# Performance work log

Measured on AMD Instinct MI355X. Metric: run time of the kernel, lower is better.

The kernel has to match this reference:

```python
import jax, jax.numpy as jnp
import numpy as np
import math

HEADS = 16
HEAD_DIM = 64
MODEL_DIM = HEADS * HEAD_DIM
SEQ = 2048
BATCH = 2


def setup_inputs() -> dict:
    key = jax.random.key(0)
    ks = jax.random.split(key, 11)
    s = 0.02
    return {
        "query": jax.random.normal(ks[0], (SEQ, BATCH, MODEL_DIM), jnp.float32),
        "key": jax.random.normal(ks[1], (SEQ, BATCH, MODEL_DIM), jnp.float32),
        "value": jax.random.normal(ks[2], (SEQ, BATCH, MODEL_DIM), jnp.float32),
        "mask": jnp.ones((1, SEQ, 1), jnp.int32),
        "Wq": jax.random.normal(ks[3], (MODEL_DIM, MODEL_DIM), jnp.float32) * s,
        "bq": jax.random.normal(ks[4], (MODEL_DIM,), jnp.float32) * s,
        "Wk": jax.random.normal(ks[5], (MODEL_DIM, MODEL_DIM), jnp.float32) * s,
        "bk": jax.random.normal(ks[6], (MODEL_DIM,), jnp.float32) * s,
        "Wv": jax.random.normal(ks[7], (MODEL_DIM, MODEL_DIM), jnp.float32) * s,
        "bv": jax.random.normal(ks[8], (MODEL_DIM,), jnp.float32) * s,
        "Wo": jax.random.normal(ks[9], (MODEL_DIM, MODEL_DIM), jnp.float32) * s,
        "bo": jax.random.normal(ks[10], (MODEL_DIM,), jnp.float32) * s,
    }


def _proj(x, W, b):
    # torch nn.Linear: y = x @ W.T + b ; then view to [.., H, D]
    y = jnp.einsum("sbm,nm->sbn", x, W) + b
    return y.reshape(x.shape[0], x.shape[1], HEADS, HEAD_DIM)


def reference(query, key, value, mask, Wq, bq, Wk, bk, Wv, bv, Wo, bo):
    # NOTE: original module applies mask to `score` AFTER softmax has been
    # taken, and the masked score is discarded -> mask has no effect.
    del mask
    seq_len, batch_size, _ = query.shape
    scale = 1.0 / math.sqrt(HEAD_DIM)
    q = _proj(query, Wq, bq)   # [S,B,H,D]
    k = _proj(key, Wk, bk)
    v = _proj(value, Wv, bv)
    score = jnp.einsum("ibhd,jbhd->ijbh", q, k) * scale  # [S,S,B,H]
    attn = jax.nn.softmax(score, axis=1)  # softmax over key axis j
    # dropout: eval-mode identity (deterministic baseline)
    x = jnp.einsum("ijbh,jbhd->ibhd", attn, v)
    x = x.reshape(seq_len, batch_size, MODEL_DIM)
    return jnp.einsum("sbm,nm->sbn", x, Wo) + bo
```

## Files before the change

### kernel.cpp

```cpp
#include <hip/hip_runtime.h>

#define SEQ    2048
#define NBATCH 2
#define NHEAD  16
#define HD     64
#define MD     1024
#define TOK    (SEQ * NBATCH)
#define WN8    (MD * MD / 8)

typedef __attribute__((ext_vector_type(4)))  float f32x4;
typedef __attribute__((ext_vector_type(16))) float f32x16;
typedef __attribute__((ext_vector_type(8)))  short bf16x8;
typedef __attribute__((ext_vector_type(8)))  unsigned short u16x8;

__device__ __forceinline__ unsigned short f2bf(float f) {
  union { float f; unsigned int u; } x; x.f = f;
  unsigned int u = x.u + 0x7fffu + ((x.u >> 16) & 1u);
  return (unsigned short)(u >> 16);
}

__device__ __forceinline__ unsigned cvtpk(float lo, float hi) {
  unsigned r;
  asm("v_cvt_pk_bf16_f32 %0, %1, %2" : "=v"(r) : "v"(lo), "v"(hi));
  return r;
}
__device__ __forceinline__ void plswap(unsigned &a, unsigned &b) {
  asm volatile("v_permlane32_swap_b32 %0, %1" : "+v"(a), "+v"(b));
}

__device__ __forceinline__ void gload_lds16(const void* g, void* l) {
  typedef const __attribute__((address_space(1))) unsigned int* gp_t;
  typedef __attribute__((address_space(3))) unsigned int* lp_t;
  __builtin_amdgcn_global_load_lds((gp_t)g, (lp_t)l, 16, 0, 0);
}

__global__ __launch_bounds__(256) void cvt_w(
    const float* __restrict__ wq, const float* __restrict__ wk,
    const float* __restrict__ wv, const float* __restrict__ wo,
    unsigned short* __restrict__ owq, unsigned short* __restrict__ owk,
    unsigned short* __restrict__ owv, unsigned short* __restrict__ owo) {
  const int i = blockIdx.x * 256 + threadIdx.x;
  const int s = i >> 17;
  const int r = i & (WN8 - 1);
  const float* src = s == 0 ? wq : (s == 1 ? wk : (s == 2 ? wv : wo));
  unsigned short* dst = s == 0 ? owq : (s == 1 ? owk : (s == 2 ? owv : owo));
  const float4* p = (const float4*)src + (size_t)r * 2;
  float4 a = p[0];
  float4 b = p[1];
  u16x8 o;
  o[0] = f2bf(a.x); o[1] = f2bf(a.y); o[2] = f2bf(a.z); o[3] = f2bf(a.w);
  o[4] = f2bf(b.x); o[5] = f2bf(b.y); o[6] = f2bf(b.z); o[7] = f2bf(b.w);
  *((u16x8*)dst + r) = o;
}

__global__ __launch_bounds__(512) void gemm_qkv(
    const float* __restrict__ Xq, const float* __restrict__ Xk,
    const float* __restrict__ Xv, const unsigned short* __restrict__ Wq,
    const unsigned short* __restrict__ Wk, const unsigned short* __restrict__ Wv,
    const float* __restrict__ bq, const float* __restrict__ bk, const float* __restrict__ bv,
    unsigned short* __restrict__ Qo, unsigned short* __restrict__ Ko,
    unsigned short* __restrict__ Vo, float qscale) {
  __shared__ unsigned short sA[3][128 * 32];
  __shared__ unsigned short sB[3][128 * 32];
  const int tid  = threadIdx.x;
  const int lane = tid & 63;
  const int wave = tid >> 6;
  const int wm   = (wave >> 2) << 6;
  const int wn   = (wave & 3) << 5;
  const int l15  = lane & 15;
  const int g    = lane >> 4;

  const int flat = blockIdx.x + (blockIdx.y << 3) + (blockIdx.z << 8);
  const int nx   = (flat & 63) >> 3;
  const int gr   = ((flat >> 6) << 3) + (flat & 7);
  const int ny   = gr & 31;
  const int z    = gr >> 5;

  const float* Xf; const unsigned short* Wb; const float* bias;
  if (z == 0)      { Xf = Xq; Wb = Wq; bias = bq; }
  else if (z == 1) { Xf = Xk; Wb = Wk; bias = bk; }
  else             { Xf = Xv; Wb = Wv; bias = bv; }
  int bM, bN;
  if (z < 2) { bM = ny << 7; bN = nx << 7; }
  else       { bM = nx << 7; bN = ny << 7; }
  const int bX = (z < 2) ? bM : bN;
  const int bW = (z < 2) ? bN : bM;
  unsigned short* sX3 = (z < 2) ? &sA[0][0] : &sB[0][0];
  unsigned short* sW3 = (z < 2) ? &sB[0][0] : &sA[0][0];

  f32x4 acc[4][2];
#pragma unroll
  for (int a_ = 0; a_ < 4; ++a_)
#pragma unroll
    for (int b_ = 0; b_ < 2; ++b_)
      acc[a_][b_] = f32x4{0.f, 0.f, 0.f, 0.f};

  const int r = tid >> 2, cc = tid & 3;
  const float* xsrc = Xf + (size_t)(bX + r) * MD + cc * 8;
  const unsigned short* wsrc = Wb + (size_t)(bW + r) * MD + cc * 8;

  float4 ra0, rb0, ra1, rb1;
  auto xissue0 = [&](int kt) {
    ra0 = *(const float4*)(xsrc + (kt << 5));
    rb0 = *(const float4*)(xsrc + (kt << 5) + 4);
  };
  auto xissue1 = [&](int kt) {
    ra1 = *(const float4*)(xsrc + (kt << 5));
    rb1 = *(const float4*)(xsrc + (kt << 5) + 4);
  };
  auto xwrite0 = [&](int c) {
    union { unsigned u[4]; bf16x8 v; } w;
    w.u[0] = cvtpk(ra0.x, ra0.y); w.u[1] = cvtpk(ra0.z, ra0.w);
    w.u[2] = cvtpk(rb0.x, rb0.y); w.u[3] = cvtpk(rb0.z, rb0.w);
    *(bf16x8*)(sX3 + c * 4096 + tid * 8) = w.v;
  };
  auto xwrite1 = [&](int c) {
    union { unsigned u[4]; bf16x8 v; } w;
    w.u[0] = cvtpk(ra1.x, ra1.y); w.u[1] = cvtpk(ra1.z, ra1.w);
    w.u[2] = cvtpk(rb1.x, rb1.y); w.u[3] = cvtpk(rb1.z, rb1.w);
    *(bf16x8*)(sX3 + c * 4096 + tid * 8) = w.v;
  };
  auto wissue = [&](int c, int kt) {
    gload_lds16(wsrc + (kt << 5), (char*)(sW3 + c * 4096) + tid * 16);
  };

  auto mfma_step = [&](int c) {
    bf16x8 af[4], bfr[2];
#pragma unroll
    for (int f = 0; f < 4; ++f)
      af[f] = *(const bf16x8*)&sA[c][(wm + f * 16 + l15) * 32 + g * 8];
#pragma unroll
    for (int f = 0; f < 2; ++f)
      bfr[f] = *(const bf16x8*)&sB[c][(wn + f * 16 + l15) * 32 + g * 8];
#pragma unroll
    for (int mf = 0; mf < 4; ++mf)
#pragma unroll
      for (int nf = 0; nf < 2; ++nf)
        acc[mf][nf] = __builtin_amdgcn_mfma_f32_16x16x32_bf16(af[mf], bfr[nf], acc[mf][nf], 0, 0, 0);
  };

  const int nk = MD >> 5;
  auto endwait = [&](int e) {
    if (e + 4 < nk)      asm volatile("s_waitcnt vmcnt(3)" ::: "memory");
    else if (e + 2 < nk) asm volatile("s_waitcnt vmcnt(1)" ::: "memory");
    else                 asm volatile("s_waitcnt vmcnt(0)" ::: "memory");
    asm volatile("s_waitcnt lgkmcnt(0)" ::: "memory");
    __builtin_amdgcn_s_barrier();
  };

  xissue0(0);
  xissue1(1);
  wissue(0, 0);
  wissue(1, 1);
  asm volatile("s_waitcnt vmcnt(4)" ::: "memory");
  xwrite0(0);
  asm volatile("s_waitcnt vmcnt(2)" ::: "memory");
  xwrite1(1);
  xissue0(2);
  xissue1(3);
  asm volatile("s_waitcnt vmcnt(4)" ::: "memory");
  asm volatile("s_waitcnt lgkmcnt(0)" ::: "memory");
  __builtin_amdgcn_s_barrier();

  for (int kt = 0; kt < nk; kt += 2) {
    if (kt + 2 < nk) { xwrite0((kt + 2) % 3); wissue((kt + 2) % 3, kt + 2); }
    if (kt + 4 < nk) xissue0(kt + 4);
    mfma_step(kt % 3);
    endwait(kt);
    if (kt + 3 < nk) { xwrite1((kt + 3) % 3); wissue((kt + 3) % 3, kt + 3); }
    if (kt + 5 < nk) xissue1(kt + 5);
    mfma_step((kt + 1) % 3);
    if (kt + 2 < nk) endwait(kt + 1);
  }

  if (z < 2) {
    unsigned short* O = (z == 0) ? Qo : Ko;
    const float scale = (z == 0) ? qscale : 1.0f;
#pragma unroll
    for (int nf = 0; nf < 2; ++nf) {
      const int cch = bN + wn + nf * 16 + l15;
      const float bb = bias[cch];
      const int h = cch >> 6, d = cch & 63;
#pragma unroll
      for (int mf = 0; mf < 4; ++mf)
#pragma unroll
        for (int i = 0; i < 4; ++i) {
          const int t = bM + wm + mf * 16 + (g << 2) + i;
          const int b = t & 1, s = t >> 1;
          O[((((b << 4) + h) * SEQ + s) << 6) + d] = f2bf((acc[mf][nf][i] + bb) * scale);
        }
    }
  } else {
#pragma unroll
    for (int mf = 0; mf < 4; ++mf)
#pragma unroll
      for (int i = 0; i < 4; ++i) {
        const int rch = bM + wm + mf * 16 + (g << 2) + i;
        const float bb = bias[rch];
        const int h = rch >> 6, d = rch & 63;
#pragma unroll
        for (int nf = 0; nf < 2; ++nf) {
          const int t = bN + wn + nf * 16 + l15;
          const int b = t & 1, s = t >> 1;
          Vo[((((b << 4) + h) << 6) + d) * SEQ + s] = f2bf(acc[mf][nf][i] + bb);
        }
      }
  }
}

__global__ __launch_bounds__(512) void gemm_oproj(const unsigned short* __restrict__ A,
                                                  const unsigned short* __restrict__ B,
                                                  const float* __restrict__ bias,
                                                  float* __restrict__ O) {
  __shared__ unsigned short sA[3][128 * 32];
  __shared__ unsigned short sB[3][128 * 32];
  const int tid  = threadIdx.x;
  const int lane = tid & 63;
  const int wave = tid >> 6;
  const int wm   = (wave >> 2) << 6;
  const int wn   = (wave & 3) << 5;
  const int l15  = lane & 15;
  const int g    = lane >> 4;

  const int flat = blockIdx.x + (blockIdx.y << 3);
  const int nx   = (flat & 63) >> 3;
  const int gr   = ((flat >> 6) << 3) + (flat & 7);
  const int bM   = gr << 7;
  const int bN   = nx << 7;

  f32x4 acc[4][2];
#pragma unroll
  for (int a_ = 0; a_ < 4; ++a_)
#pragma unroll
    for (int b_ = 0; b_ < 2; ++b_)
      acc[a_][b_] = f32x4{0.f, 0.f, 0.f, 0.f};

  const int r = tid >> 2, cc = tid & 3;
  auto stage = [&](int c, int kt) {
    const int k0 = kt << 5;
    gload_lds16(A + (size_t)(bM + r) * MD + k0 + cc * 8, (char*)sA[c] + tid * 16);
    gload_lds16(B + (size_t)(bN + r) * MD + k0 + cc * 8, (char*)sB[c] + tid * 16);
  };

  const int nk = MD >> 5;
  stage(0, 0);
  stage(1, 1);
  asm volatile("s_waitcnt vmcnt(2)" ::: "memory");
  __builtin_amdgcn_s_barrier();

  int cur = 0;
  for (int kt = 0; kt < nk; ++kt) {
    if (kt + 2 < nk) stage(cur == 0 ? 2 : cur - 1, kt + 2);
    bf16x8 af[4], bfr[2];
#pragma unroll
    for (int f = 0; f < 4; ++f)
      af[f] = *(const bf16x8*)&sA[cur][(wm + f * 16 + l15) * 32 + g * 8];
#pragma unroll
    for (int f = 0; f < 2; ++f)
      bfr[f] = *(const bf16x8*)&sB[cur][(wn + f * 16 + l15) * 32 + g * 8];
#pragma unroll
    for (int mf = 0; mf < 4; ++mf)
#pragma unroll
      for (int nf = 0; nf < 2; ++nf)
        acc[mf][nf] = __builtin_amdgcn_mfma_f32_16x16x32_bf16(af[mf], bfr[nf], acc[mf][nf], 0, 0, 0);
    if (kt + 2 < nk)
      asm volatile("s_waitcnt vmcnt(2)" ::: "memory");
    else if (kt + 1 < nk)
      asm volatile("s_waitcnt vmcnt(0)" ::: "memory");
    if (kt + 1 < nk) __builtin_amdgcn_s_barrier();
    cur = (cur == 2) ? 0 : cur + 1;
  }

#pragma unroll
  for (int nf = 0; nf < 2; ++nf) {
    const int cch = bN + wn + nf * 16 + l15;
    const float bb = bias[cch];
#pragma unroll
    for (int mf = 0; mf < 4; ++mf)
#pragma unroll
      for (int i = 0; i < 4; ++i) {
        const int t = bM + wm + mf * 16 + (g << 2) + i;
        O[(size_t)t * MD + cch] = acc[mf][nf][i] + bb;
      }
  }
}

__global__ __launch_bounds__(512) void attn_fwd(const unsigned short* __restrict__ Qg,
                                                const unsigned short* __restrict__ Kg,
                                                const unsigned short* __restrict__ Vg,
                                                unsigned short* __restrict__ Xout) {
  __shared__ unsigned short sK[2][2][64 * 64];
  __shared__ unsigned short sV[2][2][64 * 64];

  const int tid  = threadIdx.x;
  const int lane = tid & 63;
  const int wave = tid >> 6;
  const int ws   = wave & 3;
  const int grp  = wave >> 2;
  const int l31  = lane & 31;
  const int half = lane >> 5;
  const int bh   = blockIdx.y;
  const int q0w  = (blockIdx.x << 7) + (ws << 5);

  const unsigned short* Qb = Qg + (size_t)bh * (SEQ * HD);
  const char* Kb = (const char*)(Kg + (size_t)bh * (SEQ * HD));
  const char* Vb = (const char*)(Vg + (size_t)bh * (HD * SEQ));

  bf16x8 qf[4];
#pragma unroll
  for (int c = 0; c < 4; ++c)
    qf[c] = *(const bf16x8*)&Qb[(size_t)(q0w + l31) * HD + c * 16 + half * 8];

  f32x16 acc_o[2];
#pragma unroll
  for (int dt = 0; dt < 2; ++dt)
#pragma unroll
    for (int e = 0; e < 16; ++e) acc_o[dt][e] = 0.f;
  float lrow = 0.f;

  auto stage = [&](int c, int kt) {
#pragma unroll
    for (int h = 0; h < 2; ++h) {
      const int p = tid << 4;
      const int row = p >> 7;
      const int lcol = (p ^ ((row & 7) << 4)) & 127;
      const int kbase = (h << 10) + (kt << 6);
      gload_lds16(Kb + (size_t)(kbase + row) * (HD * 2) + lcol,
                  (char*)sK + ((h * 2 + c) << 13) + p);
      gload_lds16(Vb + (size_t)row * (SEQ * 2) + (kbase << 1) + lcol,
                  (char*)sV + ((h * 2 + c) << 13) + p);
    }
  };

  const char* myK = (char*)sK + (grp << 14);
  const char* myV = (char*)sV + (grp << 14);

  stage(0, 0);
  __syncthreads();
  int cur = 0;

  const int NT = SEQ / 2 / 64;
  for (int kt = 0; kt < NT; ++kt) {
    if (kt + 1 < NT) stage(cur ^ 1, kt + 1);

    f32x16 accs[2];
    __builtin_amdgcn_s_setprio(1);
#pragma unroll
    for (int ks = 0; ks < 2; ++ks) {
#pragma unroll
      for (int e = 0; e < 16; ++e) accs[ks][e] = 0.f;
      const int krow = ks * 32 + l31;
      const int swz  = (krow & 7) << 4;
#pragma unroll
      for (int c = 0; c < 4; ++c) {
        const int off = (krow << 7) + ((c * 32 + half * 16) ^ swz);
        bf16x8 kf = *(const bf16x8*)(myK + (cur << 13) + off);
        accs[ks] = __builtin_amdgcn_mfma_f32_32x32x16_bf16(kf, qf[c], accs[ks], 0, 0, 0);
      }
    }
    __builtin_amdgcn_s_setprio(0);

    float rsum = 0.f;
#pragma unroll
    for (int ks = 0; ks < 2; ++ks)
#pragma unroll
      for (int e = 0; e < 16; ++e) {
        const float pv = __builtin_amdgcn_exp2f(accs[ks][e]);
        accs[ks][e] = pv;
        rsum += pv;
      }
    lrow += rsum;

    bf16x8 pa[4];
#pragma unroll
    for (int ks = 0; ks < 2; ++ks)
#pragma unroll
      for (int hc = 0; hc < 2; ++hc) {
        const int b = hc * 8;
        unsigned X  = cvtpk(accs[ks][b + 0], accs[ks][b + 1]);
        unsigned X2 = cvtpk(accs[ks][b + 2], accs[ks][b + 3]);
        unsigned Y  = cvtpk(accs[ks][b + 4], accs[ks][b + 5]);
        unsigned Y2 = cvtpk(accs[ks][b + 6], accs[ks][b + 7]);
        plswap(X, Y);
        plswap(X2, Y2);
        union { unsigned u[4]; bf16x8 v; } w;
        w.u[0] = X; w.u[1] = X2; w.u[2] = Y; w.u[3] = Y2;
        pa[ks * 2 + hc] = w.v;
      }

    __builtin_amdgcn_s_setprio(1);
#pragma unroll
    for (int dt = 0; dt < 2; ++dt) {
      const int drow = dt * 32 + l31;
      const int swz  = (drow & 7) << 4;
#pragma unroll
      for (int kc = 0; kc < 4; ++kc) {
        const int off = (drow << 7) + ((kc * 32 + half * 16) ^ swz);
        bf16x8 vf = *(const bf16x8*)(myV + (cur << 13) + off);
        acc_o[dt] = __builtin_amdgcn_mfma_f32_32x32x16_bf16(vf, pa[kc], acc_o[dt], 0, 0, 0);
      }
    }
    __builtin_amdgcn_s_setprio(0);

    __syncthreads();
    cur ^= 1;
  }

  float lt = lrow + __shfl_xor(lrow, 32);
  float* dump  = (float*)sK;
  float* ldump = dump + 4 * 32 * 68;
  const int base = (ws * 32 + l31) * 68;

  if (grp == 1) {
#pragma unroll
    for (int dt = 0; dt < 2; ++dt)
#pragma unroll
      for (int r4 = 0; r4 < 4; ++r4) {
        const int d0 = dt * 32 + r4 * 8 + half * 4;
        const int e = r4 * 4;
        *(float2*)&dump[base + d0]     = float2{acc_o[dt][e + 0], acc_o[dt][e + 1]};
        *(float2*)&dump[base + d0 + 2] = float2{acc_o[dt][e + 2], acc_o[dt][e + 3]};
      }
    if (half == 0) ldump[ws * 32 + l31] = lt;
  }
  __syncthreads();
  if (grp == 0) {
    const float ltot = lt + ldump[ws * 32 + l31];
    const float inv = 1.f / ltot;
    const int b = bh >> 4, h = bh & 15;
    const int s = q0w + l31;
    const int t = s * NBATCH + b;
    unsigned short* Ot = Xout + (size_t)t * MD + (h << 6);
#pragma unroll
    for (int dt = 0; dt < 2; ++dt)
#pragma unroll
      for (int r4 = 0; r4 < 4; ++r4) {
        const int d0 = dt * 32 + r4 * 8 + half * 4;
        const int e = r4 * 4;
        float2 a0 = *(float2*)&dump[base + d0];
        float2 a1 = *(float2*)&dump[base + d0 + 2];
        uint2 w;
        w.x = cvtpk((acc_o[dt][e + 0] + a0.x) * inv, (acc_o[dt][e + 1] + a0.y) * inv);
        w.y = cvtpk((acc_o[dt][e + 2] + a1.x) * inv, (acc_o[dt][e + 3] + a1.y) * inv);
        *(uint2*)(Ot + d0) = w;
      }
  }
}

extern "C" void kernel_launch(void* const* d_in, const int* in_sizes, int n_in,
                              void* d_out, int out_size, void* d_ws, size_t ws_size,
                              hipStream_t stream) {
  const float* query = (const float*)d_in[0];
  const float* key   = (const float*)d_in[1];
  const float* value = (const float*)d_in[2];
  const float* Wq = (const float*)d_in[4];
  const float* bq = (const float*)d_in[5];
  const float* Wk = (const float*)d_in[6];
  const float* bk = (const float*)d_in[7];
  const float* Wv = (const float*)d_in[8];
  const float* bv = (const float*)d_in[9];
  const float* Wo = (const float*)d_in[10];
  const float* bo = (const float*)d_in[11];

  char* ws = (char*)d_ws;
  const size_t MB = 1024 * 1024;
  unsigned short* Xa  = (unsigned short*)(ws + 0 * MB);
  unsigned short* Wqb = (unsigned short*)(ws + 24 * MB);
  unsigned short* Wkb = (unsigned short*)(ws + 26 * MB);
  unsigned short* Wvb = (unsigned short*)(ws + 28 * MB);
  unsigned short* Wob = (unsigned short*)(ws + 30 * MB);
  unsigned short* Qb  = (unsigned short*)(ws + 32 * MB);
  unsigned short* Kb  = (unsigned short*)(ws + 40 * MB);
  unsigned short* Vb  = (unsigned short*)(ws + 48 * MB);

  cvt_w<<<4 * WN8 / 256, 256, 0, stream>>>(Wq, Wk, Wv, Wo, Wqb, Wkb, Wvb, Wob);

  const float kQScale = 0.125f * 1.44269504088896340736f;
  dim3 gQKV(MD / 128, TOK / 128, 3);
  gemm_qkv<<<gQKV, 512, 0, stream>>>(query, key, value, Wqb, Wkb, Wvb,
                                     bq, bk, bv, Qb, Kb, Vb, kQScale);

  dim3 gA(SEQ / 128, NBATCH * NHEAD);
  attn_fwd<<<gA, 512, 0, stream>>>(Qb, Kb, Vb, Xa);

  dim3 gO(MD / 128, TOK / 128);
  gemm_oproj<<<gO, 512, 0, stream>>>(Xa, Wob, bo, (float*)d_out);
  (void)in_sizes; (void)n_in; (void)out_size; (void)ws_size;
}
```

Baseline: 113.5 us.

## Software-pipeline attention loop: overlap PV of previous tile with QK of current

Restructures the attention inner loop so each iteration issues the QK MFMAs for tile kt together with the PV MFMAs for tile kt-1. The exp/convert work of one tile can then overlap with matrix work. V gets a triple buffer in LDS (80KB total) so the previous tile's V stays valid while the next tile loads, and a final PV step drains the pipeline. This raises LDS use, which can lower occupancy, and keeps the pa registers live across iterations.

```diff
diff --git a/kernel.cpp b/kernel.cpp
--- a/kernel.cpp
+++ b/kernel.cpp
@@ -289,8 +289,9 @@
                                                 const unsigned short* __restrict__ Kg,
                                                 const unsigned short* __restrict__ Vg,
                                                 unsigned short* __restrict__ Xout) {
-  __shared__ unsigned short sK[2][2][64 * 64];
-  __shared__ unsigned short sV[2][2][64 * 64];
+  __shared__ __align__(16) char smem[81920];
+  char* sKc = smem;
+  char* sVc = smem + 32768;
 
   const int tid  = threadIdx.x;
   const int lane = tid & 63;
@@ -318,7 +319,7 @@
     for (int e = 0; e < 16; ++e) acc_o[dt][e] = 0.f;
   float lrow = 0.f;
 
-  auto stage = [&](int c, int kt) {
+  auto stage = [&](int cK, int cV, int kt) {
 #pragma unroll
     for (int h = 0; h < 2; ++h) {
       const int p = tid << 4;
@@ -326,22 +327,23 @@
       const int lcol = (p ^ ((row & 7) << 4)) & 127;
       const int kbase = (h << 10) + (kt << 6);
       gload_lds16(Kb + (size_t)(kbase + row) * (HD * 2) + lcol,
-                  (char*)sK + ((h * 2 + c) << 13) + p);
+                  sKc + ((h * 2 + cK) << 13) + p);
       gload_lds16(Vb + (size_t)row * (SEQ * 2) + (kbase << 1) + lcol,
-                  (char*)sV + ((h * 2 + c) << 13) + p);
+                  sVc + (h * 3 + cV) * 8192 + p);
     }
   };
 
-  const char* myK = (char*)sK + (grp << 14);
-  const char* myV = (char*)sV + (grp << 14);
-
-  stage(0, 0);
+  const char* myK = sKc + (grp << 14);
+  const char* myV = sVc + grp * 3 * 8192;
+
+  stage(0, 0, 0);
   __syncthreads();
-  int cur = 0;
-
+
+  bf16x8 pa[4];
   const int NT = SEQ / 2 / 64;
+
   for (int kt = 0; kt < NT; ++kt) {
-    if (kt + 1 < NT) stage(cur ^ 1, kt + 1);
+    if (kt + 1 < NT) stage((kt + 1) & 1, (kt + 1) % 3, kt + 1);
 
     f32x16 accs[2];
     __builtin_amdgcn_s_setprio(1);
@@ -354,8 +356,22 @@
 #pragma unroll
       for (int c = 0; c < 4; ++c) {
         const int off = (krow << 7) + ((c * 32 + half * 16) ^ swz);
-        bf16x8 kf = *(const bf16x8*)(myK + (cur << 13) + off);
+        bf16x8 kf = *(const bf16x8*)(myK + ((kt & 1) << 13) + off);
         accs[ks] = __builtin_amdgcn_mfma_f32_32x32x16_bf16(kf, qf[c], accs[ks], 0, 0, 0);
+      }
+    }
+    if (kt > 0) {
+      const int vb = (kt - 1) % 3;
+#pragma unroll
+      for (int dt = 0; dt < 2; ++dt) {
+        const int drow = dt * 32 + l31;
+        const int swz  = (drow & 7) << 4;
+#pragma unroll
+        for (int kc = 0; kc < 4; ++kc) {
+          const int off = (drow << 7) + ((kc * 32 + half * 16) ^ swz);
+          bf16x8 vf = *(const bf16x8*)(myV + vb * 8192 + off);
+          acc_o[dt] = __builtin_amdgcn_mfma_f32_32x32x16_bf16(vf, pa[kc], acc_o[dt], 0, 0, 0);
+        }
       }
     }
     __builtin_amdgcn_s_setprio(0);
@@ -371,7 +387,6 @@
       }
     lrow += rsum;
 
-    bf16x8 pa[4];
 #pragma unroll
     for (int ks = 0; ks < 2; ++ks)
 #pragma unroll
@@ -388,6 +403,11 @@
         pa[ks * 2 + hc] = w.v;
       }
 
+    __syncthreads();
+  }
+
+  {
+    const int vb = (NT - 1) % 3;
     __builtin_amdgcn_s_setprio(1);
 #pragma unroll
     for (int dt = 0; dt < 2; ++dt) {
@@ -396,18 +416,16 @@
 #pragma unroll
       for (int kc = 0; kc < 4; ++kc) {
         const int off = (drow << 7) + ((kc * 32 + half * 16) ^ swz);
-        bf16x8 vf = *(const bf16x8*)(myV + (cur << 13) + off);
+        bf16x8 vf = *(const bf16x8*)(myV + vb * 8192 + off);
         acc_o[dt] = __builtin_amdgcn_mfma_f32_32x32x16_bf16(vf, pa[kc], acc_o[dt], 0, 0, 0);
       }
     }
     __builtin_amdgcn_s_setprio(0);
-
-    __syncthreads();
-    cur ^= 1;
-  }
+  }
+  __syncthreads();
 
   float lt = lrow + __shfl_xor(lrow, 32);
-  float* dump  = (float*)sK;
+  float* dump  = (float*)smem;
   float* ldump = dump + 4 * 32 * 68;
   const int base = (ws * 32 + l31) * 68;
 
```

Result: slower. 115.9 us (+2.1%).
